# Kernel optimization log

Measured on AMD Instinct MI355X. Metric: run time of the kernel, lower is better.

The kernel has to match this reference:

```python
import jax, jax.numpy as jnp
import numpy as np

# irreps config (l<=1 only)
N, E = 20000, 400000
NS, NV = 64, 32          # node: 64x0e + 32x1o  (dim 64 + 96 = 160)
ES, EV = 8, 8            # edge: 8x0e + 8x1o    (dim 8 + 24 = 32)
HS, HV = 96, 32          # hidden: 96x0e + 32x1o (last HV scalars are gates)
GS = HS - HV             # post-gate scalar channels
INV_SQRT3 = float(1.0 / np.sqrt(3.0))  # w3j(1,1,0) normalization


def _tp_gate(xs, xv, ys, yv, Wss, Wvv, Wsv, Wvs):
    """FullyConnectedTensorProduct (paths 0x0->0, 1.1->0, 0x1->1, 1x0->1)
    with fan-in path normalization, followed by a gated nonlinearity:
    silu on scalars, sigmoid-gated vectors.
    xs:[*,u] xv:[*,u',3] ys:[*,v] yv:[*,v',3] -> (gs:[*,GS], gv:[*,HV,3])"""
    n_s = 1.0 / np.sqrt(Wss.shape[0] * Wss.shape[1] + Wvv.shape[0] * Wvv.shape[1])
    n_v = 1.0 / np.sqrt(Wsv.shape[0] * Wsv.shape[1] + Wvs.shape[0] * Wvs.shape[1])
    hs = (jnp.einsum('eu,ev,uvw->ew', xs, ys, Wss)
          + INV_SQRT3 * jnp.einsum('euk,evk,uvw->ew', xv, yv, Wvv)) * n_s
    hv = (jnp.einsum('eu,evk,uvw->ewk', xs, yv, Wsv)
          + jnp.einsum('euk,ev,uvw->ewk', xv, ys, Wvs)) * n_v
    gs = jax.nn.silu(hs[:, :GS])
    gates = jax.nn.sigmoid(hs[:, GS:])          # [*, HV]
    gv = hv * gates[:, :, None]
    return gs, gv


def _irrep_linear(s, v, Ws, Wv):
    """e3nn-style Linear: independent multiplicity mixing per irrep, 1/sqrt(fan_in)."""
    return (s @ Ws) / np.sqrt(Ws.shape[0]), jnp.einsum('nuk,uw->nwk', v, Wv) / np.sqrt(Wv.shape[0])


def setup_inputs() -> dict:
    key = jax.random.key(0)
    ks = jax.random.split(key, 16)
    inp = {
        'node_features': jax.random.normal(ks[0], (N, NS + 3 * NV), jnp.float32),
        'edge_attr_tensor': jax.random.normal(ks[1], (E, ES + 3 * EV), jnp.float32),
        'node_attr_scalar_raw': jax.random.normal(ks[2], (N, 1), jnp.float32),
        'edge_index': jax.random.randint(ks[3], (2, E), 0, N),
        # message TP weights: node (x) edge -> hidden
        'W_m_ss': jax.random.normal(ks[4], (NS, ES, HS), jnp.float32),
        'W_m_vv': jax.random.normal(ks[5], (NV, EV, HS), jnp.float32),
        'W_m_sv': jax.random.normal(ks[6], (NS, EV, HV), jnp.float32),
        'W_m_vs': jax.random.normal(ks[7], (NV, ES, HV), jnp.float32),
        # linear_messages_out: gate-out (GSx0e+HVx1o) -> hidden
        'Wl_ms': jax.random.normal(ks[8], (GS, HS), jnp.float32),
        'Wl_mv': jax.random.normal(ks[9], (HV, HV), jnp.float32),
        # update TP weights: node (x) hidden -> hidden
        'W_u_ss': jax.random.normal(ks[10], (NS, HS, HS), jnp.float32),
        'W_u_vv': jax.random.normal(ks[11], (NV, HV, HS), jnp.float32),
        'W_u_sv': jax.random.normal(ks[12], (NS, HV, HV), jnp.float32),
        'W_u_vs': jax.random.normal(ks[13], (NV, HS, HV), jnp.float32),
        # linear_update_out: gate-out -> node irreps
        'Wl_us': jax.random.normal(ks[14], (GS, NS), jnp.float32),
        'Wl_uv': jax.random.normal(ks[15], (HV, NV), jnp.float32),
    }
    return inp


def reference(node_features, edge_attr_tensor, node_attr_scalar_raw, edge_index,
              W_m_ss, W_m_vv, W_m_sv, W_m_vs, Wl_ms, Wl_mv,
              W_u_ss, W_u_vv, W_u_sv, W_u_vs, Wl_us, Wl_uv):
    n = node_features.shape[0]
    row, col = edge_index[0], edge_index[1]
    xs = node_features[:, :NS]                              # [N,NS]
    xv = node_features[:, NS:].reshape(n, NV, 3)            # [N,NV,3]
    es = edge_attr_tensor[:, :ES]                           # [E,ES]
    ev = edge_attr_tensor[:, ES:].reshape(-1, EV, 3)        # [E,EV,3]
    # gather source nodes, TP with edge attrs, gate
    ms, mv = _tp_gate(xs[col], xv[col], es, ev, W_m_ss, W_m_vv, W_m_sv, W_m_vs)
    ms, mv = _irrep_linear(ms, mv, Wl_ms, Wl_mv)            # -> hidden irreps
    # scatter-sum into destination nodes
    ags = jax.ops.segment_sum(ms, row, num_segments=n)      # [N,HS]
    agv = jax.ops.segment_sum(mv.reshape(-1, HV * 3), row, num_segments=n).reshape(n, HV, 3)
    # update TP: node (x) aggregated, gate, project back to node irreps
    us, uv = _tp_gate(xs, xv, ags, agv, W_u_ss, W_u_vv, W_u_sv, W_u_vs)
    us, uv = _irrep_linear(us, uv, Wl_us, Wl_uv)
    upd = jnp.concatenate([us, uv.reshape(n, NV * 3)], axis=-1)
    return node_features + upd
```

## Files before the change

### kernel.cpp

```cpp
#include <hip/hip_runtime.h>

#define NN 20000
#define NE 400000

typedef __attribute__((ext_vector_type(4))) float f32x4;
typedef _Float16 h2 __attribute__((ext_vector_type(2)));
typedef _Float16 h8 __attribute__((ext_vector_type(8)));

union H8 { h8 v; h2 p[4]; };

__device__ __forceinline__ float sigf(float x) { return 1.0f / (1.0f + __expf(-x)); }

__device__ __forceinline__ h8 rank1(_Float16 x, const h2 e[4]) {
    h2 xb = {x, x}; H8 f;
    #pragma unroll
    for (int j = 0; j < 4; ++j) f.p[j] = xb * e[j];
    return f.v;
}
__device__ __forceinline__ h8 rank3(_Float16 x0, _Float16 x1, _Float16 x2,
                                    const h2 e0[4], const h2 e1[4], const h2 e2[4]) {
    h2 x0b = {x0, x0}, x1b = {x1, x1}, x2b = {x2, x2}; H8 f;
    #pragma unroll
    for (int j = 0; j < 4; ++j) f.p[j] = x0b * e0[j] + x1b * e1[j] + x2b * e2[j];
    return f.v;
}
#define MFMA(a, b, c) __builtin_amdgcn_mfma_f32_16x16x32_f16(a, b, c, 0, 0, 0)

__global__ __launch_bounds__(256)
void prep_kernel(const float* __restrict__ s1, const float* __restrict__ s2,
                 int K1, int Kt, int Nw, float sc1, float sc2,
                 unsigned short* __restrict__ dst)
{
    __shared__ _Float16 tile[32][34];
    const int tx = threadIdx.x & 31, ty = threadIdx.x >> 5;
    const int K0 = blockIdx.x * 32, w0 = blockIdx.y * 32;
    #pragma unroll
    for (int r = 0; r < 4; ++r) {
        int K = K0 + ty + r * 8, w = w0 + tx;
        if (K < Kt && w < Nw) {
            float v = (K < K1) ? s1[(size_t)K * Nw + w] * sc1
                               : s2[(size_t)(K - K1) * Nw + w] * sc2;
            tile[ty + r * 8][tx] = (_Float16)v;
        }
    }
    __syncthreads();
    #pragma unroll
    for (int r = 0; r < 4; ++r) {
        int w = w0 + ty + r * 8, K = K0 + tx;
        if (w < Nw && K < Kt)
            dst[(size_t)w * Kt + K] = __builtin_bit_cast(unsigned short, tile[tx][ty + r * 8]);
    }
}

__global__ void hist_kernel(const int* __restrict__ eidx, int* __restrict__ counts)
{
    int e = blockIdx.x * 256 + threadIdx.x;
    if (e < NE) atomicAdd(&counts[eidx[e]], 1);
}

__global__ __launch_bounds__(1024)
void scan_kernel(int* __restrict__ data)
{
    __shared__ int wsum[16];
    __shared__ int s_carry;
    const int t = threadIdx.x, lane = t & 63, wv = t >> 6;
    if (t == 0) s_carry = 0;
    __syncthreads();
    for (int base = 0; base < NN; base += 1024) {
        int carry = s_carry;
        int idx = base + t;
        int v = (idx < NN) ? data[idx] : 0;
        int s = v;
        #pragma unroll
        for (int d = 1; d < 64; d <<= 1) {
            int x = __shfl_up(s, d, 64);
            if (lane >= d) s += x;
        }
        if (lane == 63) wsum[wv] = s;
        __syncthreads();
        if (t < 16) {
            int ws = wsum[t];
            #pragma unroll
            for (int d = 1; d < 16; d <<= 1) {
                int x = __shfl_up(ws, d, 64);
                if (t >= d) ws += x;
            }
            wsum[t] = ws;
        }
        __syncthreads();
        if (idx < NN) data[idx] = carry + (wv ? wsum[wv - 1] : 0) + s - v;
        if (t == 0) s_carry = carry + wsum[15];
        __syncthreads();
    }
}

__global__ void scatter_kernel(const int* __restrict__ eidx, int* __restrict__ cursor,
                               int* __restrict__ perm)
{
    int e = blockIdx.x * 256 + threadIdx.x;
    if (e < NE) {
        int r = eidx[e];
        int p = atomicAdd(&cursor[r], 1);
        perm[p] = e;
    }
}

template<int MB>
__device__ __forceinline__ void msg_gemmB(
    int ln, int okt,
    const _Float16 (*s_xsh)[68], const _Float16 (*s_xv01)[66], const _Float16 (*s_xv2)[34],
    const _Float16 (*s_esh)[8], const _Float16 (*s_evTh)[3][8],
    const unsigned short* __restrict__ wB, f32x4* acc)
{
    const unsigned short* b0p = wB + (size_t)ln * 768;
    const unsigned short* b1p = wB + (size_t)(16 + ln) * 768;

    h2 vv[6][4];
    #pragma unroll
    for (int m = 0; m < 6; ++m) {
        const int k = (MB + m) >> 2, e = (((MB + m) & 3) << 4) + ln;
        #pragma unroll
        for (int j = 0; j < 4; ++j) vv[m][j] = ((const h2*)s_evTh[e][k])[j];
    }
    #pragma unroll 4
    for (int ks = 0; ks < 16; ++ks) {
        const int ko = ks * 32 + okt * 8, u = ks * 4 + okt;
        h8 b0 = *(const h8*)(b0p + ko), b1 = *(const h8*)(b1p + ko);
        #pragma unroll
        for (int m = 0; m < 6; ++m) {
            const int e = (((MB + m) & 3) << 4) + ln;
            h8 a = rank1(s_xsh[e][u], vv[m]);
            acc[m * 2]     = MFMA(a, b0, acc[m * 2]);
            acc[m * 2 + 1] = MFMA(a, b1, acc[m * 2 + 1]);
        }
    }
    h2 ee[6][4];
    #pragma unroll
    for (int m = 0; m < 6; ++m) {
        const int e = (((MB + m) & 3) << 4) + ln;
        #pragma unroll
        for (int j = 0; j < 4; ++j) ee[m][j] = ((const h2*)s_esh[e])[j];
    }
    #pragma unroll 4
    for (int ks = 0; ks < 8; ++ks) {
        const int ko = 512 + ks * 32 + okt * 8, u = ks * 4 + okt;
        h8 b0 = *(const h8*)(b0p + ko), b1 = *(const h8*)(b1p + ko);
        #pragma unroll
        for (int m = 0; m < 6; ++m) {
            const int k = (MB + m) >> 2, e = (((MB + m) & 3) << 4) + ln;
            _Float16 x = (k < 2) ? s_xv01[e][u * 2 + k] : s_xv2[e][u];
            h8 a = rank1(x, ee[m]);
            acc[m * 2]     = MFMA(a, b0, acc[m * 2]);
            acc[m * 2 + 1] = MFMA(a, b1, acc[m * 2 + 1]);
        }
    }
}

__global__ __launch_bounds__(256, 3)
void msg_kernel(const float* __restrict__ nf, const float* __restrict__ ea,
                const int* __restrict__ eidx, const int* __restrict__ perm,
                const unsigned short* __restrict__ wA,
                const unsigned short* __restrict__ wB,
                float* __restrict__ agg)
{
    const int e0 = blockIdx.x * 64;
    const int t = threadIdx.x;
    const int wid = t >> 6, lane = t & 63, ln = lane & 15, okt = lane >> 4;

    __shared__ __align__(16) char smem[25600];
    _Float16 (*s_xsh)[68]    = (_Float16(*)[68])(smem);
    _Float16 (*s_xv01)[66]   = (_Float16(*)[66])(smem + 8704);
    _Float16 (*s_xv2)[34]    = (_Float16(*)[34])(smem + 17152);
    _Float16 (*s_esh)[8]     = (_Float16(*)[8])(smem + 21504);
    _Float16 (*s_evTh)[3][8] = (_Float16(*)[3][8])(smem + 22528);
    _Float16 (*s_msg)[162]   = (_Float16(*)[162])(smem);
    _Float16 (*s_gate)[33]   = (_Float16(*)[33])(smem + 20736);

    __shared__ int s_row[64], s_col[64], s_pe[64];

    if (t < 64) {
        int p = perm[e0 + t];
        s_pe[t] = p;
        s_row[t] = eidx[p];
        s_col[t] = eidx[NE + p];
    }
    __syncthreads();
    for (int i = t; i < 64 * 32; i += 256) {
        int e = i >> 5, c = i & 31;
        float v = ea[(size_t)s_pe[e] * 32 + c];
        if (c < 8) s_esh[e][c] = (_Float16)v;
        else { int d = c - 8; s_evTh[e][d % 3][d / 3] = (_Float16)v; }
    }
    for (int i = t; i < 64 * 40; i += 256) {
        int e = i / 40, q = i - e * 40;
        f32x4 f4 = *((const f32x4*)nf + (size_t)s_col[e] * 40 + q);
        if (q < 16) {
            #pragma unroll
            for (int j = 0; j < 4; ++j) s_xsh[e][q * 4 + j] = (_Float16)f4[j];
        } else {
            #pragma unroll
            for (int j = 0; j < 4; ++j) {
                int d = (q - 16) * 4 + j, u = d / 3, k = d - u * 3;
                if (k < 2) s_xv01[e][u * 2 + k] = (_Float16)f4[j];
                else       s_xv2[e][u] = (_Float16)f4[j];
            }
        }
    }
    __syncthreads();

    f32x4 acc[12] = {};

    if (wid < 2) {
        const unsigned short* wb = wA + (size_t)(wid * 48 + ln) * 768;
        h2 esv[4][4];
        #pragma unroll
        for (int m = 0; m < 4; ++m)
            #pragma unroll
            for (int j = 0; j < 4; ++j) esv[m][j] = ((const h2*)s_esh[m * 16 + ln])[j];
        #pragma unroll 4
        for (int ks = 0; ks < 16; ++ks) {
            const int ko = ks * 32 + okt * 8, u = ks * 4 + okt;
            h8 b0 = *(const h8*)(wb + ko);
            h8 b1 = *(const h8*)(wb + 16 * 768 + ko);
            h8 b2 = *(const h8*)(wb + 32 * 768 + ko);
            #pragma unroll
            for (int m = 0; m < 4; ++m) {
                h8 a = rank1(s_xsh[m * 16 + ln][u], esv[m]);
                acc[m * 3 + 0] = MFMA(a, b0, acc[m * 3 + 0]);
                acc[m * 3 + 1] = MFMA(a, b1, acc[m * 3 + 1]);
                acc[m * 3 + 2] = MFMA(a, b2, acc[m * 3 + 2]);
            }
        }
        h2 ev0[4][4], ev1[4][4], ev2[4][4];
        #pragma unroll
        for (int m = 0; m < 4; ++m)
            #pragma unroll
            for (int j = 0; j < 4; ++j) {
                ev0[m][j] = ((const h2*)s_evTh[m * 16 + ln][0])[j];
                ev1[m][j] = ((const h2*)s_evTh[m * 16 + ln][1])[j];
                ev2[m][j] = ((const h2*)s_evTh[m * 16 + ln][2])[j];
            }
        #pragma unroll 4
        for (int ks = 0; ks < 8; ++ks) {
            const int ko = 512 + ks * 32 + okt * 8, u = ks * 4 + okt;
            h8 b0 = *(const h8*)(wb + ko);
            h8 b1 = *(const h8*)(wb + 16 * 768 + ko);
            h8 b2 = *(const h8*)(wb + 32 * 768 + ko);
            #pragma unroll
            for (int m = 0; m < 4; ++m) {
                h2 x01 = *(const h2*)&s_xv01[m * 16 + ln][u * 2];
                h8 a = rank3(x01[0], x01[1], s_xv2[m * 16 + ln][u], ev0[m], ev1[m], ev2[m]);
                acc[m * 3 + 0] = MFMA(a, b0, acc[m * 3 + 0]);
                acc[m * 3 + 1] = MFMA(a, b1, acc[m * 3 + 1]);
                acc[m * 3 + 2] = MFMA(a, b2, acc[m * 3 + 2]);
            }
        }
    } else if (wid == 2) {
        msg_gemmB<0>(ln, okt, s_xsh, s_xv01, s_xv2, s_esh, s_evTh, wB, acc);
    } else {
        msg_gemmB<6>(ln, okt, s_xsh, s_xv01, s_xv2, s_esh, s_evTh, wB, acc);
    }

    __syncthreads();

    if (wid < 2) {
        #pragma unroll
        for (int m = 0; m < 4; ++m)
            #pragma unroll
            for (int j = 0; j < 3; ++j)
                #pragma unroll
                for (int r = 0; r < 4; ++r) {
                    int e = m * 16 + okt * 4 + r;
                    int w = wid * 48 + j * 16 + ln;
                    float h = acc[m * 3 + j][r];
                    if (w < 64) s_msg[e][w] = (_Float16)(h * sigf(h));
                    else        s_gate[e][w - 64] = (_Float16)sigf(h);
                }
    }
    __syncthreads();
    if (wid >= 2) {
        const int mb = (wid - 2) * 6;
        #pragma unroll
        for (int m = 0; m < 6; ++m) {
            int mm = mb + m, k = mm >> 2;
            #pragma unroll
            for (int tt = 0; tt < 2; ++tt)
                #pragma unroll
                for (int r = 0; r < 4; ++r) {
                    int e = ((mm & 3) << 4) + okt * 4 + r;
                    int w2 = tt * 16 + ln;
                    s_msg[e][64 + w2 * 3 + k] =
                        (_Float16)(acc[m * 2 + tt][r] * (float)s_gate[e][w2]);
                }
        }
    }
    __syncthreads();

    if (t < 160) {
        int cur = s_row[0];
        float a = (float)s_msg[0][t];
        for (int e = 1; e < 64; ++e) {
            int r = s_row[e];
            float v = (float)s_msg[e][t];
            if (r != cur) {
                atomicAdd(agg + (size_t)cur * 160 + t, a);
                cur = r; a = v;
            } else a += v;
        }
        atomicAdd(agg + (size_t)cur * 160 + t, a);
    }
}

__global__ __launch_bounds__(256, 3)
void upd_kernel(const float* __restrict__ nf, const float* __restrict__ agg,
                const unsigned short* __restrict__ wA,
                const unsigned short* __restrict__ wB,
                const float* __restrict__ Wlms, const float* __restrict__ Wlmv,
                const float* __restrict__ Wls, const float* __restrict__ Wlv,
                float* __restrict__ out)
{
    const int n0 = blockIdx.x * 32;
    const int t = threadIdx.x;
    const int wid = t >> 6, lane = t & 63, ln = lane & 15, okt = lane >> 4;

    __shared__ __align__(16) _Float16 s_xsh[32][68];
    __shared__ __align__(16) _Float16 s_xv01[32][66];
    __shared__ __align__(16) _Float16 s_xv2[32][34];
    __shared__ __align__(16) _Float16 s_ash[32][104];
    __shared__ __align__(16) _Float16 s_avTh[32][3][40];
    __shared__ _Float16 s_hs2[32][104];
    __shared__ _Float16 s_hv2[96][34];

    for (int i = t; i < 32 * 40; i += 256) {
        int n = i / 40, q = i - n * 40;
        f32x4 f4 = *((const f32x4*)nf + (size_t)(n0 + n) * 40 + q);
        if (q < 16) {
            #pragma unroll
            for (int j = 0; j < 4; ++j) s_xsh[n][q * 4 + j] = (_Float16)f4[j];
        } else {
            #pragma unroll
            for (int j = 0; j < 4; ++j) {
                int d = (q - 16) * 4 + j, u = d / 3, k = d - u * 3;
                if (k < 2) s_xv01[n][u * 2 + k] = (_Float16)f4[j];
                else       s_xv2[n][u] = (_Float16)f4[j];
            }
        }
    }
    const float* agr = agg + (size_t)n0 * 160;
    #pragma unroll
    for (int r = 0; r < 12; ++r) {
        int o = t + r * 256;
        int n = o / 96, q = o - n * 96;
        float a = 0.f;
        #pragma unroll
        for (int u = 0; u < 64; ++u) a = fmaf(agr[n * 160 + u], Wlms[u * 96 + q], a);
        s_ash[n][q] = (_Float16)(a * 0.125f);
    }
    #pragma unroll
    for (int r = 0; r < 12; ++r) {
        int o = t + r * 256;
        int n = o / 96, q = o - n * 96, k = q >> 5, v = q & 31;
        float a = 0.f;
        #pragma unroll
        for (int u = 0; u < 32; ++u) a = fmaf(agr[n * 160 + 64 + u * 3 + k], Wlmv[u * 32 + v], a);
        s_avTh[n][k][v] = (_Float16)(a * 0.17677669529663687f);
    }
    __syncthreads();

    f32x4 acc[6] = {};

    if (wid < 2) {
        const unsigned short* wb = wA + (size_t)(wid * 48 + ln) * 7168;
        #pragma unroll 2
        for (int kb = 0; kb < 64; ++kb) {
            _Float16 x0 = s_xsh[ln][kb];
            _Float16 x1 = s_xsh[16 + ln][kb];
            #pragma unroll
            for (int p = 0; p < 3; ++p) {
                const int ko = kb * 96 + p * 32 + okt * 8;
                const int v0 = p * 32 + okt * 8;
                h8 b0 = *(const h8*)(wb + ko);
                h8 b1 = *(const h8*)(wb + 16 * 7168 + ko);
                h8 b2 = *(const h8*)(wb + 32 * 7168 + ko);
                h8 a0 = rank1(x0, (const h2*)&s_ash[ln][v0]);
                h8 a1 = rank1(x1, (const h2*)&s_ash[16 + ln][v0]);
                acc[0] = MFMA(a0, b0, acc[0]); acc[1] = MFMA(a0, b1, acc[1]); acc[2] = MFMA(a0, b2, acc[2]);
                acc[3] = MFMA(a1, b0, acc[3]); acc[4] = MFMA(a1, b1, acc[4]); acc[5] = MFMA(a1, b2, acc[5]);
            }
        }
        #pragma unroll 4
        for (int ks = 0; ks < 32; ++ks) {
            const int ko = 6144 + ks * 32 + okt * 8;
            const int v0 = okt * 8;
            h8 b0 = *(const h8*)(wb + ko);
            h8 b1 = *(const h8*)(wb + 16 * 7168 + ko);
            h8 b2 = *(const h8*)(wb + 32 * 7168 + ko);
            h2 xa = *(const h2*)&s_xv01[ln][ks * 2];
            h2 xb = *(const h2*)&s_xv01[16 + ln][ks * 2];
            h8 a0 = rank3(xa[0], xa[1], s_xv2[ln][ks],
                          (const h2*)&s_avTh[ln][0][v0], (const h2*)&s_avTh[ln][1][v0],
                          (const h2*)&s_avTh[ln][2][v0]);
            h8 a1 = rank3(xb[0], xb[1], s_xv2[16 + ln][ks],
                          (const h2*)&s_avTh[16 + ln][0][v0], (const h2*)&s_avTh[16 + ln][1][v0],
                          (const h2*)&s_avTh[16 + ln][2][v0]);
            acc[0] = MFMA(a0, b0, acc[0]); acc[1] = MFMA(a0, b1, acc[1]); acc[2] = MFMA(a0, b2, acc[2]);
            acc[3] = MFMA(a1, b0, acc[3]); acc[4] = MFMA(a1, b1, acc[4]); acc[5] = MFMA(a1, b2, acc[5]);
        }
    } else {
        const unsigned short* bp = wB + (size_t)((wid - 2) * 16 + ln) * 5120;
        #pragma unroll 2
        for (int ks = 0; ks < 64; ++ks) {
            const int ko = ks * 32 + okt * 8;
            const int v0 = okt * 8;
            h8 b = *(const h8*)(bp + ko);
            #pragma unroll
            for (int m = 0; m < 6; ++m) {
                const int k = m >> 1, n = ((m & 1) << 4) + ln;
                h8 a = rank1(s_xsh[n][ks], (const h2*)&s_avTh[n][k][v0]);
                acc[m] = MFMA(a, b, acc[m]);
            }
        }
        #pragma unroll 2
        for (int kb = 0; kb < 32; ++kb) {
            _Float16 xa[6];
            #pragma unroll
            for (int m = 0; m < 6; ++m) {
                const int k = m >> 1, n = ((m & 1) << 4) + ln;
                xa[m] = (k < 2) ? s_xv01[n][kb * 2 + k] : s_xv2[n][kb];
            }
            #pragma unroll
            for (int p = 0; p < 3; ++p) {
                const int ko = 2048 + kb * 96 + p * 32 + okt * 8;
                const int v0 = p * 32 + okt * 8;
                h8 b = *(const h8*)(bp + ko);
                #pragma unroll
                for (int m = 0; m < 6; ++m) {
                    const int n = ((m & 1) << 4) + ln;
                    h8 a = rank1(xa[m], (const h2*)&s_ash[n][v0]);
                    acc[m] = MFMA(a, b, acc[m]);
                }
            }
        }
    }

    if (wid < 2) {
        #pragma unroll
        for (int m = 0; m < 2; ++m)
            #pragma unroll
            for (int j = 0; j < 3; ++j)
                #pragma unroll
                for (int r = 0; r < 4; ++r)
                    s_hs2[m * 16 + okt * 4 + r][wid * 48 + j * 16 + ln] = (_Float16)acc[m * 3 + j][r];
    } else {
        #pragma unroll
        for (int m = 0; m < 6; ++m)
            #pragma unroll
            for (int r = 0; r < 4; ++r)
                s_hv2[m * 16 + okt * 4 + r][(wid - 2) * 16 + ln] = (_Float16)acc[m][r];
    }
    __syncthreads();
    for (int i = t; i < 32 * 96; i += 256) {
        int n = i / 96, w = i - n * 96;
        float h = (float)s_hs2[n][w];
        s_hs2[n][w] = (_Float16)((w < 64) ? h * sigf(h) : sigf(h));
    }
    __syncthreads();
    for (int i = t; i < 96 * 32; i += 256) {
        int R = i >> 5, w2 = i & 31, n = R & 31;
        s_hv2[R][w2] = (_Float16)((float)s_hv2[R][w2] * (float)s_hs2[n][64 + w2]);
    }
    __syncthreads();
    for (int i = t; i < 32 * 64; i += 256) {
        int n = i >> 6, w = i & 63;
        float a = 0.f;
        #pragma unroll
        for (int u = 0; u < 64; ++u) a = fmaf((float)s_hs2[n][u], Wls[u * 64 + w], a);
        size_t o = (size_t)(n0 + n) * 160 + w;
        out[o] = nf[o] + a * 0.125f;
    }
    for (int i = t; i < 32 * 96; i += 256) {
        int n = i / 96, wk = i - n * 96, w = wk / 3, k = wk - w * 3;
        float a = 0.f;
        #pragma unroll
        for (int u = 0; u < 32; ++u) a = fmaf((float)s_hv2[k * 32 + n][u], Wlv[u * 32 + w], a);
        size_t o = (size_t)(n0 + n) * 160 + 64 + wk;
        out[o] = nf[o] + a * 0.17677669529663687f;
    }
}

extern "C" void kernel_launch(void* const* d_in, const int* in_sizes, int n_in,
                              void* d_out, int out_size, void* d_ws, size_t ws_size,
                              hipStream_t stream) {
    const float* nf   = (const float*)d_in[0];
    const float* ea   = (const float*)d_in[1];
    const int*   eidx = (const int*)d_in[3];
    const float* Wmss = (const float*)d_in[4];
    const float* Wmvv = (const float*)d_in[5];
    const float* Wmsv = (const float*)d_in[6];
    const float* Wmvs = (const float*)d_in[7];
    const float* Wlms = (const float*)d_in[8];
    const float* Wlmv = (const float*)d_in[9];
    const float* Wuss = (const float*)d_in[10];
    const float* Wuvv = (const float*)d_in[11];
    const float* Wusv = (const float*)d_in[12];
    const float* Wuvs = (const float*)d_in[13];
    const float* Wlus = (const float*)d_in[14];
    const float* Wluv = (const float*)d_in[15];
    float* out = (float*)d_out;

    float* agg = (float*)d_ws;
    unsigned short* wAm = (unsigned short*)(agg + (size_t)NN * 160);
    unsigned short* wBm = wAm + 96 * 768;
    unsigned short* wAu = wBm + 32 * 768;
    unsigned short* wBu = wAu + (size_t)96 * 7168;
    int* counts = (int*)(wBu + (size_t)32 * 5120);
    int* perm   = counts + NN;

    const float NSM = 0.03608439182435161f;
    const float NSU = 0.011811365506297619f;
    const float NVU = 0.013975424859373686f;
    const float S3  = 0.57735026918962576f;

    hipMemsetAsync(agg, 0, (size_t)NN * 160 * sizeof(float), stream);
    hipMemsetAsync(counts, 0, (size_t)NN * sizeof(int), stream);

    prep_kernel<<<dim3(24, 3), 256, 0, stream>>>(Wmss, Wmvv, 512, 768, 96, NSM, NSM * S3, wAm);
    prep_kernel<<<dim3(24, 1), 256, 0, stream>>>(Wmsv, Wmvs, 512, 768, 32, NSM, NSM, wBm);
    prep_kernel<<<dim3(224, 3), 256, 0, stream>>>(Wuss, Wuvv, 6144, 7168, 96, NSU, NSU * S3, wAu);
    prep_kernel<<<dim3(160, 1), 256, 0, stream>>>(Wusv, Wuvs, 2048, 5120, 32, NVU, NVU, wBu);

    hist_kernel<<<(NE + 255) / 256, 256, 0, stream>>>(eidx, counts);
    scan_kernel<<<1, 1024, 0, stream>>>(counts);
    scatter_kernel<<<(NE + 255) / 256, 256, 0, stream>>>(eidx, counts, perm);

    msg_kernel<<<NE / 64, 256, 0, stream>>>(nf, ea, eidx, perm, wAm, wBm, agg);
    upd_kernel<<<NN / 32, 256, 0, stream>>>(nf, agg, wAu, wBu, Wlms, Wlmv, Wlus, Wluv, out);
}
```

Baseline: 582.0 us.

## Double msg_kernel tile to 128 edges with 512 threads and 8 waves

The message kernel now processes 128 edges per block using 8 waves instead of 64 edges with 4. Four waves split the scalar/gate GEMM over two edge halves and two column halves, and four waves cover the vector GEMM's 24 row tiles. The shared-memory layout doubles, and the segmented atomic reduction runs in two halves of 64 edges. The intent is to amortise per-block overhead and weight loads over more edges. In exchange it uses twice the LDS per block and lowers blocks per CU.

After: 715.2 us. 1.23x slower.

```diff
diff --git a/kernel.cpp b/kernel.cpp
--- a/kernel.cpp
+++ b/kernel.cpp
@@ -118,7 +118,7 @@
     h2 vv[6][4];
     #pragma unroll
     for (int m = 0; m < 6; ++m) {
-        const int k = (MB + m) >> 2, e = (((MB + m) & 3) << 4) + ln;
+        const int k = (MB + m) >> 3, e = (((MB + m) & 7) << 4) + ln;
         #pragma unroll
         for (int j = 0; j < 4; ++j) vv[m][j] = ((const h2*)s_evTh[e][k])[j];
     }
@@ -128,7 +128,7 @@
         h8 b0 = *(const h8*)(b0p + ko), b1 = *(const h8*)(b1p + ko);
         #pragma unroll
         for (int m = 0; m < 6; ++m) {
-            const int e = (((MB + m) & 3) << 4) + ln;
+            const int e = (((MB + m) & 7) << 4) + ln;
             h8 a = rank1(s_xsh[e][u], vv[m]);
             acc[m * 2]     = MFMA(a, b0, acc[m * 2]);
             acc[m * 2 + 1] = MFMA(a, b1, acc[m * 2 + 1]);
@@ -137,7 +137,7 @@
     h2 ee[6][4];
     #pragma unroll
     for (int m = 0; m < 6; ++m) {
-        const int e = (((MB + m) & 3) << 4) + ln;
+        const int e = (((MB + m) & 7) << 4) + ln;
         #pragma unroll
         for (int j = 0; j < 4; ++j) ee[m][j] = ((const h2*)s_esh[e])[j];
     }
@@ -147,7 +147,7 @@
         h8 b0 = *(const h8*)(b0p + ko), b1 = *(const h8*)(b1p + ko);
         #pragma unroll
         for (int m = 0; m < 6; ++m) {
-            const int k = (MB + m) >> 2, e = (((MB + m) & 3) << 4) + ln;
+            const int k = (MB + m) >> 3, e = (((MB + m) & 7) << 4) + ln;
             _Float16 x = (k < 2) ? s_xv01[e][u * 2 + k] : s_xv2[e][u];
             h8 a = rank1(x, ee[m]);
             acc[m * 2]     = MFMA(a, b0, acc[m * 2]);
@@ -156,42 +156,42 @@
     }
 }
 
-__global__ __launch_bounds__(256, 3)
+__global__ __launch_bounds__(512, 2)
 void msg_kernel(const float* __restrict__ nf, const float* __restrict__ ea,
                 const int* __restrict__ eidx, const int* __restrict__ perm,
                 const unsigned short* __restrict__ wA,
                 const unsigned short* __restrict__ wB,
                 float* __restrict__ agg)
 {
-    const int e0 = blockIdx.x * 64;
+    const int e0 = blockIdx.x * 128;
     const int t = threadIdx.x;
     const int wid = t >> 6, lane = t & 63, ln = lane & 15, okt = lane >> 4;
 
-    __shared__ __align__(16) char smem[25600];
+    __shared__ __align__(16) char smem[51200];
     _Float16 (*s_xsh)[68]    = (_Float16(*)[68])(smem);
-    _Float16 (*s_xv01)[66]   = (_Float16(*)[66])(smem + 8704);
-    _Float16 (*s_xv2)[34]    = (_Float16(*)[34])(smem + 17152);
-    _Float16 (*s_esh)[8]     = (_Float16(*)[8])(smem + 21504);
-    _Float16 (*s_evTh)[3][8] = (_Float16(*)[3][8])(smem + 22528);
+    _Float16 (*s_xv01)[66]   = (_Float16(*)[66])(smem + 17408);
+    _Float16 (*s_xv2)[34]    = (_Float16(*)[34])(smem + 34304);
+    _Float16 (*s_esh)[8]     = (_Float16(*)[8])(smem + 43008);
+    _Float16 (*s_evTh)[3][8] = (_Float16(*)[3][8])(smem + 45056);
     _Float16 (*s_msg)[162]   = (_Float16(*)[162])(smem);
-    _Float16 (*s_gate)[33]   = (_Float16(*)[33])(smem + 20736);
-
-    __shared__ int s_row[64], s_col[64], s_pe[64];
-
-    if (t < 64) {
+    _Float16 (*s_gate)[33]   = (_Float16(*)[33])(smem + 41472);
+
+    __shared__ int s_row[128], s_col[128], s_pe[128];
+
+    if (t < 128) {
         int p = perm[e0 + t];
         s_pe[t] = p;
         s_row[t] = eidx[p];
         s_col[t] = eidx[NE + p];
     }
     __syncthreads();
-    for (int i = t; i < 64 * 32; i += 256) {
+    for (int i = t; i < 128 * 32; i += 512) {
         int e = i >> 5, c = i & 31;
         float v = ea[(size_t)s_pe[e] * 32 + c];
         if (c < 8) s_esh[e][c] = (_Float16)v;
         else { int d = c - 8; s_evTh[e][d % 3][d / 3] = (_Float16)v; }
     }
-    for (int i = t; i < 64 * 40; i += 256) {
+    for (int i = t; i < 128 * 40; i += 512) {
         int e = i / 40, q = i - e * 40;
         f32x4 f4 = *((const f32x4*)nf + (size_t)s_col[e] * 40 + q);
         if (q < 16) {
@@ -210,13 +210,15 @@
 
     f32x4 acc[12] = {};
 
-    if (wid < 2) {
-        const unsigned short* wb = wA + (size_t)(wid * 48 + ln) * 768;
+    if (wid < 4) {
+        const int mh = wid >> 1, nh = wid & 1;
+        const int eb = mh * 64;
+        const unsigned short* wb = wA + (size_t)(nh * 48 + ln) * 768;
         h2 esv[4][4];
         #pragma unroll
         for (int m = 0; m < 4; ++m)
             #pragma unroll
-            for (int j = 0; j < 4; ++j) esv[m][j] = ((const h2*)s_esh[m * 16 + ln])[j];
+            for (int j = 0; j < 4; ++j) esv[m][j] = ((const h2*)s_esh[eb + m * 16 + ln])[j];
         #pragma unroll 4
         for (int ks = 0; ks < 16; ++ks) {
             const int ko = ks * 32 + okt * 8, u = ks * 4 + okt;
@@ -225,7 +227,7 @@
             h8 b2 = *(const h8*)(wb + 32 * 768 + ko);
             #pragma unroll
             for (int m = 0; m < 4; ++m) {
-                h8 a = rank1(s_xsh[m * 16 + ln][u], esv[m]);
+                h8 a = rank1(s_xsh[eb + m * 16 + ln][u], esv[m]);
                 acc[m * 3 + 0] = MFMA(a, b0, acc[m * 3 + 0]);
                 acc[m * 3 + 1] = MFMA(a, b1, acc[m * 3 + 1]);
                 acc[m * 3 + 2] = MFMA(a, b2, acc[m * 3 + 2]);
@@ -236,9 +238,9 @@
         for (int m = 0; m < 4; ++m)
             #pragma unroll
             for (int j = 0; j < 4; ++j) {
-                ev0[m][j] = ((const h2*)s_evTh[m * 16 + ln][0])[j];
-                ev1[m][j] = ((const h2*)s_evTh[m * 16 + ln][1])[j];
-                ev2[m][j] = ((const h2*)s_evTh[m * 16 + ln][2])[j];
+                ev0[m][j] = ((const h2*)s_evTh[eb + m * 16 + ln][0])[j];
+                ev1[m][j] = ((const h2*)s_evTh[eb + m * 16 + ln][1])[j];
+                ev2[m][j] = ((const h2*)s_evTh[eb + m * 16 + ln][2])[j];
             }
         #pragma unroll 4
         for (int ks = 0; ks < 8; ++ks) {
@@ -248,46 +250,51 @@
             h8 b2 = *(const h8*)(wb + 32 * 768 + ko);
             #pragma unroll
             for (int m = 0; m < 4; ++m) {
-                h2 x01 = *(const h2*)&s_xv01[m * 16 + ln][u * 2];
-                h8 a = rank3(x01[0], x01[1], s_xv2[m * 16 + ln][u], ev0[m], ev1[m], ev2[m]);
+                h2 x01 = *(const h2*)&s_xv01[eb + m * 16 + ln][u * 2];
+                h8 a = rank3(x01[0], x01[1], s_xv2[eb + m * 16 + ln][u], ev0[m], ev1[m], ev2[m]);
                 acc[m * 3 + 0] = MFMA(a, b0, acc[m * 3 + 0]);
                 acc[m * 3 + 1] = MFMA(a, b1, acc[m * 3 + 1]);
                 acc[m * 3 + 2] = MFMA(a, b2, acc[m * 3 + 2]);
             }
         }
-    } else if (wid == 2) {
+    } else if (wid == 4) {
         msg_gemmB<0>(ln, okt, s_xsh, s_xv01, s_xv2, s_esh, s_evTh, wB, acc);
+    } else if (wid == 5) {
+        msg_gemmB<6>(ln, okt, s_xsh, s_xv01, s_xv2, s_esh, s_evTh, wB, acc);
+    } else if (wid == 6) {
+        msg_gemmB<12>(ln, okt, s_xsh, s_xv01, s_xv2, s_esh, s_evTh, wB, acc);
     } else {
-        msg_gemmB<6>(ln, okt, s_xsh, s_xv01, s_xv2, s_esh, s_evTh, wB, acc);
-    }
-
-    __syncthreads();
-
-    if (wid < 2) {
+        msg_gemmB<18>(ln, okt, s_xsh, s_xv01, s_xv2, s_esh, s_evTh, wB, acc);
+    }
+
+    __syncthreads();
+
+    if (wid < 4) {
+        const int mh = wid >> 1, nh = wid & 1;
         #pragma unroll
         for (int m = 0; m < 4; ++m)
             #pragma unroll
             for (int j = 0; j < 3; ++j)
                 #pragma unroll
                 for (int r = 0; r < 4; ++r) {
-                    int e = m * 16 + okt * 4 + r;
-                    int w = wid * 48 + j * 16 + ln;
+                    int e = mh * 64 + m * 16 + okt * 4 + r;
+                    int w = nh * 48 + j * 16 + ln;
                     float h = acc[m * 3 + j][r];
                     if (w < 64) s_msg[e][w] = (_Float16)(h * sigf(h));
                     else        s_gate[e][w - 64] = (_Float16)sigf(h);
                 }
     }
     __syncthreads();
-    if (wid >= 2) {
-        const int mb = (wid - 2) * 6;
+    if (wid >= 4) {
+        const int MB = (wid - 4) * 6;
         #pragma unroll
         for (int m = 0; m < 6; ++m) {
-            int mm = mb + m, k = mm >> 2;
+            int mt = MB + m, k = mt >> 3;
             #pragma unroll
             for (int tt = 0; tt < 2; ++tt)
                 #pragma unroll
                 for (int r = 0; r < 4; ++r) {
-                    int e = ((mm & 3) << 4) + okt * 4 + r;
+                    int e = ((mt & 7) << 4) + okt * 4 + r;
                     int w2 = tt * 16 + ln;
                     s_msg[e][64 + w2 * 3 + k] =
                         (_Float16)(acc[m * 2 + tt][r] * (float)s_gate[e][w2]);
@@ -296,18 +303,21 @@
     }
     __syncthreads();
 
-    if (t < 160) {
-        int cur = s_row[0];
-        float a = (float)s_msg[0][t];
-        for (int e = 1; e < 64; ++e) {
+    if (t < 320) {
+        int h = (t >= 160) ? 1 : 0;
+        int c = t - h * 160;
+        int eb = h * 64;
+        int cur = s_row[eb];
+        float a = (float)s_msg[eb][c];
+        for (int e = eb + 1; e < eb + 64; ++e) {
             int r = s_row[e];
-            float v = (float)s_msg[e][t];
+            float v = (float)s_msg[e][c];
             if (r != cur) {
-                atomicAdd(agg + (size_t)cur * 160 + t, a);
+                atomicAdd(agg + (size_t)cur * 160 + c, a);
                 cur = r; a = v;
             } else a += v;
         }
-        atomicAdd(agg + (size_t)cur * 160 + t, a);
+        atomicAdd(agg + (size_t)cur * 160 + c, a);
     }
 }
 
@@ -533,6 +543,6 @@
     scan_kernel<<<1, 1024, 0, stream>>>(counts);
     scatter_kernel<<<(NE + 255) / 256, 256, 0, stream>>>(eidx, counts, perm);
 
-    msg_kernel<<<NE / 64, 256, 0, stream>>>(nf, ea, eidx, perm, wAm, wBm, agg);
+    msg_kernel<<<NE / 128, 512, 0, stream>>>(nf, ea, eidx, perm, wAm, wBm, agg);
     upd_kernel<<<NN / 32, 256, 0, stream>>>(nf, agg, wAu, wBu, Wlms, Wlmv, Wlus, Wluv, out);
 }
```

## Switch message-kernel GEMMs from 16x16x32 to 32x32x16 MFMA tiles

Applied to the files above, without the earlier changes.

Replaces the 16x16x32 f16 MFMA tiling in the message kernel with 32x32x16 MFMA. The A and B fragment layouts, the per-wave edge and channel assignment, and the epilogue index mapping for gating and vector outputs all change to match. Larger tiles mean fewer rank1/rank3 fragment constructions and fewer B loads per FLOP, cutting VALU and LDS overhead around the matrix ops. In exchange, accumulators move to 16-wide vectors, which can change register pressure and occupancy.

Result: slower. 729.2 us (+25.3%).

```diff
diff --git a/kernel.cpp b/kernel.cpp
--- a/kernel.cpp
+++ b/kernel.cpp
@@ -4,6 +4,7 @@
 #define NE 400000
 
 typedef __attribute__((ext_vector_type(4))) float f32x4;
+typedef __attribute__((ext_vector_type(16))) float f32x16;
 typedef _Float16 h2 __attribute__((ext_vector_type(2)));
 typedef _Float16 h8 __attribute__((ext_vector_type(8)));
 
@@ -25,6 +26,7 @@
     return f.v;
 }
 #define MFMA(a, b, c) __builtin_amdgcn_mfma_f32_16x16x32_f16(a, b, c, 0, 0, 0)
+#define MFMA32(a, b, c) __builtin_amdgcn_mfma_f32_32x32x16_f16(a, b, c, 0, 0, 0)
 
 __global__ __launch_bounds__(256)
 void prep_kernel(const float* __restrict__ s1, const float* __restrict__ s2,
@@ -106,52 +108,46 @@
 }
 
 template<int MB>
-__device__ __forceinline__ void msg_gemmB(
-    int ln, int okt,
+__device__ __forceinline__ void msg_gemmB32(
+    int l31, int kh,
     const _Float16 (*s_xsh)[68], const _Float16 (*s_xv01)[66], const _Float16 (*s_xv2)[34],
     const _Float16 (*s_esh)[8], const _Float16 (*s_evTh)[3][8],
-    const unsigned short* __restrict__ wB, f32x4* acc)
-{
-    const unsigned short* b0p = wB + (size_t)ln * 768;
-    const unsigned short* b1p = wB + (size_t)(16 + ln) * 768;
-
-    h2 vv[6][4];
-    #pragma unroll
-    for (int m = 0; m < 6; ++m) {
-        const int k = (MB + m) >> 2, e = (((MB + m) & 3) << 4) + ln;
-        #pragma unroll
-        for (int j = 0; j < 4; ++j) vv[m][j] = ((const h2*)s_evTh[e][k])[j];
-    }
-    #pragma unroll 4
-    for (int ks = 0; ks < 16; ++ks) {
-        const int ko = ks * 32 + okt * 8, u = ks * 4 + okt;
-        h8 b0 = *(const h8*)(b0p + ko), b1 = *(const h8*)(b1p + ko);
-        #pragma unroll
-        for (int m = 0; m < 6; ++m) {
-            const int e = (((MB + m) & 3) << 4) + ln;
-            h8 a = rank1(s_xsh[e][u], vv[m]);
-            acc[m * 2]     = MFMA(a, b0, acc[m * 2]);
-            acc[m * 2 + 1] = MFMA(a, b1, acc[m * 2 + 1]);
-        }
-    }
-    h2 ee[6][4];
-    #pragma unroll
-    for (int m = 0; m < 6; ++m) {
-        const int e = (((MB + m) & 3) << 4) + ln;
-        #pragma unroll
-        for (int j = 0; j < 4; ++j) ee[m][j] = ((const h2*)s_esh[e])[j];
-    }
-    #pragma unroll 4
-    for (int ks = 0; ks < 8; ++ks) {
-        const int ko = 512 + ks * 32 + okt * 8, u = ks * 4 + okt;
-        h8 b0 = *(const h8*)(b0p + ko), b1 = *(const h8*)(b1p + ko);
-        #pragma unroll
-        for (int m = 0; m < 6; ++m) {
-            const int k = (MB + m) >> 2, e = (((MB + m) & 3) << 4) + ln;
-            _Float16 x = (k < 2) ? s_xv01[e][u * 2 + k] : s_xv2[e][u];
-            h8 a = rank1(x, ee[m]);
-            acc[m * 2]     = MFMA(a, b0, acc[m * 2]);
-            acc[m * 2 + 1] = MFMA(a, b1, acc[m * 2 + 1]);
+    const unsigned short* __restrict__ wB, f32x16* acc)
+{
+    const unsigned short* wb = wB + (size_t)l31 * 768 + kh * 8;
+
+    h2 evk[3][4], esv[3][4];
+    int em[3];
+    #pragma unroll
+    for (int m = 0; m < 3; ++m) {
+        const int mt = MB + m, k = mt >> 1;
+        em[m] = ((mt & 1) << 5) + l31;
+        #pragma unroll
+        for (int j = 0; j < 4; ++j) {
+            evk[m][j] = ((const h2*)s_evTh[em[m]][k])[j];
+            esv[m][j] = ((const h2*)s_esh[em[m]])[j];
+        }
+    }
+    #pragma unroll 8
+    for (int s = 0; s < 32; ++s) {
+        const int u = 2 * s + kh;
+        h8 b = *(const h8*)(wb + s * 16);
+        #pragma unroll
+        for (int m = 0; m < 3; ++m) {
+            h8 a = rank1(s_xsh[em[m]][u], evk[m]);
+            acc[m] = MFMA32(a, b, acc[m]);
+        }
+    }
+    #pragma unroll 8
+    for (int s = 0; s < 16; ++s) {
+        const int u = 2 * s + kh;
+        h8 b = *(const h8*)(wb + 512 + s * 16);
+        #pragma unroll
+        for (int m = 0; m < 3; ++m) {
+            const int k = (MB + m) >> 1;
+            _Float16 x = (k < 2) ? s_xv01[em[m]][u * 2 + k] : s_xv2[em[m]][u];
+            h8 a = rank1(x, esv[m]);
+            acc[m] = MFMA32(a, b, acc[m]);
         }
     }
 }
@@ -165,7 +161,8 @@
 {
     const int e0 = blockIdx.x * 64;
     const int t = threadIdx.x;
-    const int wid = t >> 6, lane = t & 63, ln = lane & 15, okt = lane >> 4;
+    const int wid = t >> 6, lane = t & 63;
+    const int l31 = lane & 31, kh = lane >> 5;
 
     __shared__ __align__(16) char smem[25600];
     _Float16 (*s_xsh)[68]    = (_Float16(*)[68])(smem);
@@ -208,90 +205,71 @@
     }
     __syncthreads();
 
-    f32x4 acc[12] = {};
+    f32x16 acc[3] = {};
 
     if (wid < 2) {
-        const unsigned short* wb = wA + (size_t)(wid * 48 + ln) * 768;
-        h2 esv[4][4];
-        #pragma unroll
-        for (int m = 0; m < 4; ++m)
-            #pragma unroll
-            for (int j = 0; j < 4; ++j) esv[m][j] = ((const h2*)s_esh[m * 16 + ln])[j];
-        #pragma unroll 4
-        for (int ks = 0; ks < 16; ++ks) {
-            const int ko = ks * 32 + okt * 8, u = ks * 4 + okt;
-            h8 b0 = *(const h8*)(wb + ko);
-            h8 b1 = *(const h8*)(wb + 16 * 768 + ko);
-            h8 b2 = *(const h8*)(wb + 32 * 768 + ko);
-            #pragma unroll
-            for (int m = 0; m < 4; ++m) {
-                h8 a = rank1(s_xsh[m * 16 + ln][u], esv[m]);
-                acc[m * 3 + 0] = MFMA(a, b0, acc[m * 3 + 0]);
-                acc[m * 3 + 1] = MFMA(a, b1, acc[m * 3 + 1]);
-                acc[m * 3 + 2] = MFMA(a, b2, acc[m * 3 + 2]);
-            }
-        }
-        h2 ev0[4][4], ev1[4][4], ev2[4][4];
-        #pragma unroll
-        for (int m = 0; m < 4; ++m)
-            #pragma unroll
-            for (int j = 0; j < 4; ++j) {
-                ev0[m][j] = ((const h2*)s_evTh[m * 16 + ln][0])[j];
-                ev1[m][j] = ((const h2*)s_evTh[m * 16 + ln][1])[j];
-                ev2[m][j] = ((const h2*)s_evTh[m * 16 + ln][2])[j];
-            }
-        #pragma unroll 4
-        for (int ks = 0; ks < 8; ++ks) {
-            const int ko = 512 + ks * 32 + okt * 8, u = ks * 4 + okt;
-            h8 b0 = *(const h8*)(wb + ko);
-            h8 b1 = *(const h8*)(wb + 16 * 768 + ko);
-            h8 b2 = *(const h8*)(wb + 32 * 768 + ko);
-            #pragma unroll
-            for (int m = 0; m < 4; ++m) {
-                h2 x01 = *(const h2*)&s_xv01[m * 16 + ln][u * 2];
-                h8 a = rank3(x01[0], x01[1], s_xv2[m * 16 + ln][u], ev0[m], ev1[m], ev2[m]);
-                acc[m * 3 + 0] = MFMA(a, b0, acc[m * 3 + 0]);
-                acc[m * 3 + 1] = MFMA(a, b1, acc[m * 3 + 1]);
-                acc[m * 3 + 2] = MFMA(a, b2, acc[m * 3 + 2]);
-            }
+        const int e = wid * 32 + l31;
+        const unsigned short* wb0 = wA + (size_t)l31 * 768 + kh * 8;
+        const unsigned short* wb1 = wb0 + (size_t)32 * 768;
+        const unsigned short* wb2 = wb0 + (size_t)64 * 768;
+        h2 esv[4], ev0[4], ev1[4], ev2[4];
+        #pragma unroll
+        for (int j = 0; j < 4; ++j) {
+            esv[j] = ((const h2*)s_esh[e])[j];
+            ev0[j] = ((const h2*)s_evTh[e][0])[j];
+            ev1[j] = ((const h2*)s_evTh[e][1])[j];
+            ev2[j] = ((const h2*)s_evTh[e][2])[j];
+        }
+        #pragma unroll 8
+        for (int s = 0; s < 32; ++s) {
+            const int u = 2 * s + kh;
+            h8 a = rank1(s_xsh[e][u], esv);
+            acc[0] = MFMA32(a, *(const h8*)(wb0 + s * 16), acc[0]);
+            acc[1] = MFMA32(a, *(const h8*)(wb1 + s * 16), acc[1]);
+            acc[2] = MFMA32(a, *(const h8*)(wb2 + s * 16), acc[2]);
+        }
+        #pragma unroll 8
+        for (int s = 0; s < 16; ++s) {
+            const int u = 2 * s + kh;
+            h2 x01 = *(const h2*)&s_xv01[e][u * 2];
+            h8 a = rank3(x01[0], x01[1], s_xv2[e][u], ev0, ev1, ev2);
+            acc[0] = MFMA32(a, *(const h8*)(wb0 + 512 + s * 16), acc[0]);
+            acc[1] = MFMA32(a, *(const h8*)(wb1 + 512 + s * 16), acc[1]);
+            acc[2] = MFMA32(a, *(const h8*)(wb2 + 512 + s * 16), acc[2]);
         }
     } else if (wid == 2) {
-        msg_gemmB<0>(ln, okt, s_xsh, s_xv01, s_xv2, s_esh, s_evTh, wB, acc);
+        msg_gemmB32<0>(l31, kh, s_xsh, s_xv01, s_xv2, s_esh, s_evTh, wB, acc);
     } else {
-        msg_gemmB<6>(ln, okt, s_xsh, s_xv01, s_xv2, s_esh, s_evTh, wB, acc);
+        msg_gemmB32<3>(l31, kh, s_xsh, s_xv01, s_xv2, s_esh, s_evTh, wB, acc);
     }
 
     __syncthreads();
 
     if (wid < 2) {
         #pragma unroll
-        for (int m = 0; m < 4; ++m)
-            #pragma unroll
-            for (int j = 0; j < 3; ++j)
-                #pragma unroll
-                for (int r = 0; r < 4; ++r) {
-                    int e = m * 16 + okt * 4 + r;
-                    int w = wid * 48 + j * 16 + ln;
-                    float h = acc[m * 3 + j][r];
-                    if (w < 64) s_msg[e][w] = (_Float16)(h * sigf(h));
-                    else        s_gate[e][w - 64] = (_Float16)sigf(h);
-                }
+        for (int n = 0; n < 3; ++n)
+            #pragma unroll
+            for (int j = 0; j < 16; ++j) {
+                int e = wid * 32 + (j & 3) + 8 * (j >> 2) + 4 * kh;
+                int w = n * 32 + l31;
+                float h = acc[n][j];
+                if (w < 64) s_msg[e][w] = (_Float16)(h * sigf(h));
+                else        s_gate[e][w - 64] = (_Float16)sigf(h);
+            }
     }
     __syncthreads();
     if (wid >= 2) {
-        const int mb = (wid - 2) * 6;
-        #pragma unroll
-        for (int m = 0; m < 6; ++m) {
-            int mm = mb + m, k = mm >> 2;
-            #pragma unroll
-            for (int tt = 0; tt < 2; ++tt)
-                #pragma unroll
-                for (int r = 0; r < 4; ++r) {
-                    int e = ((mm & 3) << 4) + okt * 4 + r;
-                    int w2 = tt * 16 + ln;
-                    s_msg[e][64 + w2 * 3 + k] =
-                        (_Float16)(acc[m * 2 + tt][r] * (float)s_gate[e][w2]);
-                }
+        const int MB = (wid - 2) * 3;
+        #pragma unroll
+        for (int m = 0; m < 3; ++m) {
+            const int mt = MB + m, k = mt >> 1;
+            #pragma unroll
+            for (int j = 0; j < 16; ++j) {
+                int r = (j & 3) + 8 * (j >> 2) + 4 * kh;
+                int e = ((mt & 1) << 5) + r;
+                s_msg[e][64 + l31 * 3 + k] =
+                    (_Float16)(acc[m][j] * (float)s_gate[e][l31]);
+            }
         }
     }
     __syncthreads();
```

## Split update tensor-product reduction into two K-halves with a separate epilogue kernel

Applied to the files above, without the earlier changes.

The update kernel is split into two launches, each covering about half of the reduction dimension, and the partial results are written in fp32 to a workspace buffer. A third kernel sums the two partials and then applies the gate, the final irrep linear and the residual. The goal is to cut per-block serial work, balance the wave workloads, and raise occupancy by allowing 4 blocks per CU. The cost is extra global traffic for the partial buffer, two more launches, and the aggregated-input projection being recomputed in both halves.

New measurement: 653.7 us. +12.3%, slower.

```diff
diff --git a/kernel.cpp b/kernel.cpp
--- a/kernel.cpp
+++ b/kernel.cpp
@@ -311,13 +311,13 @@
     }
 }
 
-__global__ __launch_bounds__(256, 3)
-void upd_kernel(const float* __restrict__ nf, const float* __restrict__ agg,
-                const unsigned short* __restrict__ wA,
-                const unsigned short* __restrict__ wB,
-                const float* __restrict__ Wlms, const float* __restrict__ Wlmv,
-                const float* __restrict__ Wls, const float* __restrict__ Wlv,
-                float* __restrict__ out)
+template<int KH>
+__global__ __launch_bounds__(256, 4)
+void upd1_kernel(const float* __restrict__ nf, const float* __restrict__ agg,
+                 const unsigned short* __restrict__ wA,
+                 const unsigned short* __restrict__ wB,
+                 const float* __restrict__ Wlms, const float* __restrict__ Wlmv,
+                 float* __restrict__ hpart)
 {
     const int n0 = blockIdx.x * 32;
     const int t = threadIdx.x;
@@ -328,8 +328,6 @@
     __shared__ __align__(16) _Float16 s_xv2[32][34];
     __shared__ __align__(16) _Float16 s_ash[32][104];
     __shared__ __align__(16) _Float16 s_avTh[32][3][40];
-    __shared__ _Float16 s_hs2[32][104];
-    __shared__ _Float16 s_hv2[96][34];
 
     for (int i = t; i < 32 * 40; i += 256) {
         int n = i / 40, q = i - n * 40;
@@ -368,11 +366,13 @@
     __syncthreads();
 
     f32x4 acc[6] = {};
+    constexpr int KB0 = KH ? 37 : 0;
+    constexpr int KB1 = KH ? 64 : 37;
 
     if (wid < 2) {
         const unsigned short* wb = wA + (size_t)(wid * 48 + ln) * 7168;
         #pragma unroll 2
-        for (int kb = 0; kb < 64; ++kb) {
+        for (int kb = KB0; kb < KB1; ++kb) {
             _Float16 x0 = s_xsh[ln][kb];
             _Float16 x1 = s_xsh[16 + ln][kb];
             #pragma unroll
@@ -388,93 +388,123 @@
                 acc[3] = MFMA(a1, b0, acc[3]); acc[4] = MFMA(a1, b1, acc[4]); acc[5] = MFMA(a1, b2, acc[5]);
             }
         }
-        #pragma unroll 4
-        for (int ks = 0; ks < 32; ++ks) {
-            const int ko = 6144 + ks * 32 + okt * 8;
-            const int v0 = okt * 8;
-            h8 b0 = *(const h8*)(wb + ko);
-            h8 b1 = *(const h8*)(wb + 16 * 7168 + ko);
-            h8 b2 = *(const h8*)(wb + 32 * 7168 + ko);
-            h2 xa = *(const h2*)&s_xv01[ln][ks * 2];
-            h2 xb = *(const h2*)&s_xv01[16 + ln][ks * 2];
-            h8 a0 = rank3(xa[0], xa[1], s_xv2[ln][ks],
-                          (const h2*)&s_avTh[ln][0][v0], (const h2*)&s_avTh[ln][1][v0],
-                          (const h2*)&s_avTh[ln][2][v0]);
-            h8 a1 = rank3(xb[0], xb[1], s_xv2[16 + ln][ks],
-                          (const h2*)&s_avTh[16 + ln][0][v0], (const h2*)&s_avTh[16 + ln][1][v0],
-                          (const h2*)&s_avTh[16 + ln][2][v0]);
-            acc[0] = MFMA(a0, b0, acc[0]); acc[1] = MFMA(a0, b1, acc[1]); acc[2] = MFMA(a0, b2, acc[2]);
-            acc[3] = MFMA(a1, b0, acc[3]); acc[4] = MFMA(a1, b1, acc[4]); acc[5] = MFMA(a1, b2, acc[5]);
+        if (KH) {
+            #pragma unroll 4
+            for (int ks = 0; ks < 32; ++ks) {
+                const int ko = 6144 + ks * 32 + okt * 8;
+                const int v0 = okt * 8;
+                h8 b0 = *(const h8*)(wb + ko);
+                h8 b1 = *(const h8*)(wb + 16 * 7168 + ko);
+                h8 b2 = *(const h8*)(wb + 32 * 7168 + ko);
+                h2 xa = *(const h2*)&s_xv01[ln][ks * 2];
+                h2 xb = *(const h2*)&s_xv01[16 + ln][ks * 2];
+                h8 a0 = rank3(xa[0], xa[1], s_xv2[ln][ks],
+                              (const h2*)&s_avTh[ln][0][v0], (const h2*)&s_avTh[ln][1][v0],
+                              (const h2*)&s_avTh[ln][2][v0]);
+                h8 a1 = rank3(xb[0], xb[1], s_xv2[16 + ln][ks],
+                              (const h2*)&s_avTh[16 + ln][0][v0], (const h2*)&s_avTh[16 + ln][1][v0],
+                              (const h2*)&s_avTh[16 + ln][2][v0]);
+                acc[0] = MFMA(a0, b0, acc[0]); acc[1] = MFMA(a0, b1, acc[1]); acc[2] = MFMA(a0, b2, acc[2]);
+                acc[3] = MFMA(a1, b0, acc[3]); acc[4] = MFMA(a1, b1, acc[4]); acc[5] = MFMA(a1, b2, acc[5]);
+            }
         }
     } else {
         const unsigned short* bp = wB + (size_t)((wid - 2) * 16 + ln) * 5120;
-        #pragma unroll 2
-        for (int ks = 0; ks < 64; ++ks) {
-            const int ko = ks * 32 + okt * 8;
-            const int v0 = okt * 8;
-            h8 b = *(const h8*)(bp + ko);
-            #pragma unroll
-            for (int m = 0; m < 6; ++m) {
-                const int k = m >> 1, n = ((m & 1) << 4) + ln;
-                h8 a = rank1(s_xsh[n][ks], (const h2*)&s_avTh[n][k][v0]);
-                acc[m] = MFMA(a, b, acc[m]);
-            }
-        }
-        #pragma unroll 2
-        for (int kb = 0; kb < 32; ++kb) {
-            _Float16 xa[6];
-            #pragma unroll
-            for (int m = 0; m < 6; ++m) {
-                const int k = m >> 1, n = ((m & 1) << 4) + ln;
-                xa[m] = (k < 2) ? s_xv01[n][kb * 2 + k] : s_xv2[n][kb];
-            }
-            #pragma unroll
-            for (int p = 0; p < 3; ++p) {
-                const int ko = 2048 + kb * 96 + p * 32 + okt * 8;
-                const int v0 = p * 32 + okt * 8;
+        if (!KH) {
+            #pragma unroll 2
+            for (int ks = 0; ks < 64; ++ks) {
+                const int ko = ks * 32 + okt * 8;
+                const int v0 = okt * 8;
                 h8 b = *(const h8*)(bp + ko);
                 #pragma unroll
                 for (int m = 0; m < 6; ++m) {
-                    const int n = ((m & 1) << 4) + ln;
-                    h8 a = rank1(xa[m], (const h2*)&s_ash[n][v0]);
+                    const int k = m >> 1, n = ((m & 1) << 4) + ln;
+                    h8 a = rank1(s_xsh[n][ks], (const h2*)&s_avTh[n][k][v0]);
                     acc[m] = MFMA(a, b, acc[m]);
                 }
             }
-        }
-    }
-
+        } else {
+            #pragma unroll 2
+            for (int kb = 0; kb < 32; ++kb) {
+                _Float16 xa[6];
+                #pragma unroll
+                for (int m = 0; m < 6; ++m) {
+                    const int k = m >> 1, n = ((m & 1) << 4) + ln;
+                    xa[m] = (k < 2) ? s_xv01[n][kb * 2 + k] : s_xv2[n][kb];
+                }
+                #pragma unroll
+                for (int p = 0; p < 3; ++p) {
+                    const int ko = 2048 + kb * 96 + p * 32 + okt * 8;
+                    const int v0 = p * 32 + okt * 8;
+                    h8 b = *(const h8*)(bp + ko);
+                    #pragma unroll
+                    for (int m = 0; m < 6; ++m) {
+                        const int n = ((m & 1) << 4) + ln;
+                        h8 a = rank1(xa[m], (const h2*)&s_ash[n][v0]);
+                        acc[m] = MFMA(a, b, acc[m]);
+                    }
+                }
+            }
+        }
+    }
+
+    float* hp = hpart + ((size_t)KH * NN + n0) * 192;
     if (wid < 2) {
         #pragma unroll
         for (int m = 0; m < 2; ++m)
             #pragma unroll
             for (int j = 0; j < 3; ++j)
                 #pragma unroll
-                for (int r = 0; r < 4; ++r)
-                    s_hs2[m * 16 + okt * 4 + r][wid * 48 + j * 16 + ln] = (_Float16)acc[m * 3 + j][r];
+                for (int r = 0; r < 4; ++r) {
+                    int n = m * 16 + okt * 4 + r;
+                    int w = wid * 48 + j * 16 + ln;
+                    hp[(size_t)n * 192 + w] = acc[m * 3 + j][r];
+                }
     } else {
         #pragma unroll
         for (int m = 0; m < 6; ++m)
             #pragma unroll
-            for (int r = 0; r < 4; ++r)
-                s_hv2[m * 16 + okt * 4 + r][(wid - 2) * 16 + ln] = (_Float16)acc[m][r];
+            for (int r = 0; r < 4; ++r) {
+                int R = m * 16 + okt * 4 + r;
+                int k = R >> 5, n = R & 31;
+                int w2 = (wid - 2) * 16 + ln;
+                hp[(size_t)n * 192 + 96 + w2 * 3 + k] = acc[m][r];
+            }
+    }
+}
+
+__global__ __launch_bounds__(256)
+void upd2_kernel(const float* __restrict__ nf, const float* __restrict__ hpart,
+                 const float* __restrict__ Wls, const float* __restrict__ Wlv,
+                 float* __restrict__ out)
+{
+    const int n0 = blockIdx.x * 32;
+    const int t = threadIdx.x;
+    __shared__ float s_h[32][194];
+
+    const float* h0 = hpart + (size_t)n0 * 192;
+    const float* h1 = hpart + ((size_t)NN + n0) * 192;
+    for (int i = t; i < 32 * 192; i += 256) {
+        int n = i / 192, c = i - n * 192;
+        s_h[n][c] = h0[(size_t)n * 192 + c] + h1[(size_t)n * 192 + c];
     }
     __syncthreads();
     for (int i = t; i < 32 * 96; i += 256) {
         int n = i / 96, w = i - n * 96;
-        float h = (float)s_hs2[n][w];
-        s_hs2[n][w] = (_Float16)((w < 64) ? h * sigf(h) : sigf(h));
-    }
-    __syncthreads();
-    for (int i = t; i < 96 * 32; i += 256) {
-        int R = i >> 5, w2 = i & 31, n = R & 31;
-        s_hv2[R][w2] = (_Float16)((float)s_hv2[R][w2] * (float)s_hs2[n][64 + w2]);
+        float h = s_h[n][w];
+        s_h[n][w] = (w < 64) ? h * sigf(h) : sigf(h);
+    }
+    __syncthreads();
+    for (int i = t; i < 32 * 96; i += 256) {
+        int n = i / 96, wk = i - n * 96, w2 = wk / 3;
+        s_h[n][96 + wk] *= s_h[n][64 + w2];
     }
     __syncthreads();
     for (int i = t; i < 32 * 64; i += 256) {
         int n = i >> 6, w = i & 63;
         float a = 0.f;
         #pragma unroll
-        for (int u = 0; u < 64; ++u) a = fmaf((float)s_hs2[n][u], Wls[u * 64 + w], a);
+        for (int u = 0; u < 64; ++u) a = fmaf(s_h[n][u], Wls[u * 64 + w], a);
         size_t o = (size_t)(n0 + n) * 160 + w;
         out[o] = nf[o] + a * 0.125f;
     }
@@ -482,7 +512,7 @@
         int n = i / 96, wk = i - n * 96, w = wk / 3, k = wk - w * 3;
         float a = 0.f;
         #pragma unroll
-        for (int u = 0; u < 32; ++u) a = fmaf((float)s_hv2[k * 32 + n][u], Wlv[u * 32 + w], a);
+        for (int u = 0; u < 32; ++u) a = fmaf(s_h[n][96 + u * 3 + k], Wlv[u * 32 + w], a);
         size_t o = (size_t)(n0 + n) * 160 + 64 + wk;
         out[o] = nf[o] + a * 0.17677669529663687f;
     }
@@ -515,6 +545,7 @@
     unsigned short* wBu = wAu + (size_t)96 * 7168;
     int* counts = (int*)(wBu + (size_t)32 * 5120);
     int* perm   = counts + NN;
+    float* hpart = (float*)(perm + NE);
 
     const float NSM = 0.03608439182435161f;
     const float NSU = 0.011811365506297619f;
@@ -534,5 +565,8 @@
     scatter_kernel<<<(NE + 255) / 256, 256, 0, stream>>>(eidx, counts, perm);
 
     msg_kernel<<<NE / 64, 256, 0, stream>>>(nf, ea, eidx, perm, wAm, wBm, agg);
-    upd_kernel<<<NN / 32, 256, 0, stream>>>(nf, agg, wAu, wBu, Wlms, Wlmv, Wlus, Wluv, out);
-}
+
+    upd1_kernel<0><<<NN / 32, 256, 0, stream>>>(nf, agg, wAu, wBu, Wlms, Wlmv, hpart);
+    upd1_kernel<1><<<NN / 32, 256, 0, stream>>>(nf, agg, wAu, wBu, Wlms, Wlmv, hpart);
+    upd2_kernel<<<NN / 32, 256, 0, stream>>>(nf, hpart, Wlus, Wluv, out);
+}
```
